# Performance work log

Measured on AMD Instinct MI355X. Metric: run time of the kernel, lower is better.

Reference implementation:

```python
import jax, jax.numpy as jnp
import numpy as np


def setup_inputs() -> dict:
    key0 = jax.random.key(0)
    kq, kk, kv = jax.random.split(key0, 3)
    B, H, L, S, D = 2, 8, 2048, 2048, 64
    query = jax.random.normal(kq, (B, H, L, D), dtype=jnp.float32)
    key = jax.random.normal(kk, (B, H, S, D), dtype=jnp.float32)
    value = jax.random.normal(kv, (B, H, S, D), dtype=jnp.float32)
    return {"query": query, "key": key, "value": value}


def reference(query, key, value):
    # Original computes matmul(q[b,h,l,1,d,1], k[b,h,1,s,1,d]) -> [B,H,L,S,D,D]
    # outer products, divides by sqrt(query.shape[-1]) AFTER unsqueeze (==1, no-op),
    # then sums dims (4,5). That is algebraically exactly rowsum(q)*rowsum(k).
    qsum = query.sum(axis=-1)                       # [B,H,L]
    ksum = key.sum(axis=-1)                         # [B,H,S]
    score = qsum[..., :, None] * ksum[..., None, :]  # [B,H,L,S]
    attn = jax.nn.softmax(score, axis=-1)            # softmax over S
    out = jnp.einsum('bhls,bhsd->bhld', attn, value)  # [B,H,L,D]
    return out
```

## Files before the change

kernel.cpp:

```cpp
#include <hip/hip_runtime.h>
#include <hip/hip_bf16.h>

#define BH 16
#define L 2048
#define S 2048
#define DD 64
#define BM 64
#define BK 64
#define LDSPAD 8
#define LDW (BK + LDSPAD)

typedef __attribute__((ext_vector_type(4))) float f32x4;
typedef __bf16 bf16x8 __attribute__((ext_vector_type(8)));

union FragU {
  bf16x8 f;
  __hip_bfloat162 h2[4];
};

__device__ inline __hip_bfloat162 exp2pack(float al2, float nsl2, float k0,
                                           float k1, float& d) {
  float e0 = __builtin_amdgcn_exp2f(fmaf(al2, k0, nsl2));
  float e1 = __builtin_amdgcn_exp2f(fmaf(al2, k1, nsl2));
  d += e0 + e1;
  return __float22bfloat162_rn(make_float2(e0, e1));
}

__global__ __launch_bounds__(256) void prep_kernel(
    const float* __restrict__ k, const float* __restrict__ v,
    float* __restrict__ ks, __hip_bfloat16* __restrict__ vt) {
  __shared__ __hip_bfloat16 tile[DD][LDW];
  int t = threadIdx.x;
  if (blockIdx.x < 2048) {
    int g = blockIdx.x * 256 + t;
    int row = g >> 4;
    int l16 = g & 15;
    float4 x = reinterpret_cast<const float4*>(k + (size_t)row * DD)[l16];
    float s = x.x + x.y + x.z + x.w;
    s += __shfl_xor(s, 1);
    s += __shfl_xor(s, 2);
    s += __shfl_xor(s, 4);
    s += __shfl_xor(s, 8);
    if (l16 == 0) ks[row] = s;
  } else {
    int bid = blockIdx.x - 2048;
    int s0 = (bid & 31) * 64;
    int bh = bid >> 5;
    int srow = t >> 4;
    int d4 = (t & 15) * 4;
#pragma unroll
    for (int kk = 0; kk < 4; ++kk) {
      int s = srow + kk * 16;
      float4 val = *reinterpret_cast<const float4*>(
          v + ((size_t)(bh * S + s0 + s)) * DD + d4);
      tile[d4 + 0][s] = __float2bfloat16(val.x);
      tile[d4 + 1][s] = __float2bfloat16(val.y);
      tile[d4 + 2][s] = __float2bfloat16(val.z);
      tile[d4 + 3][s] = __float2bfloat16(val.w);
    }
    __syncthreads();
    int dd = t >> 3;
    int j = t & 7;
#pragma unroll
    for (int kk = 0; kk < 2; ++kk) {
      int d = dd + kk * 32;
      uint4 val = *reinterpret_cast<const uint4*>(&tile[d][j * 8]);
      *reinterpret_cast<uint4*>(vt + ((size_t)(bh * DD + d)) * S + s0 + j * 8) =
          val;
    }
  }
}

__global__ __launch_bounds__(256) void attn_kernel(
    const float* __restrict__ q, const __hip_bfloat16* __restrict__ vt,
    const float* __restrict__ ks, float* __restrict__ out) {
  int l0 = blockIdx.x * BM;
  int bh = blockIdx.y;

  __shared__ __hip_bfloat16 ldsVT[2][DD][LDW];
  __shared__ float a_row[BM];
  __shared__ float red[16];

  int t = threadIdx.x;
  int lane = t & 63;
  int w = t >> 6;
  int m = lane & 15;
  int qd = lane >> 4;

  const __hip_bfloat16* vtb = vt + (size_t)bh * DD * S;
  const float* ksb = ks + (size_t)bh * S;

  int vd = t >> 3;
  int vj = t & 7;

  uint4 v0 = *reinterpret_cast<const uint4*>(vtb + (size_t)vd * S + vj * 8);
  uint4 v1 =
      *reinterpret_cast<const uint4*>(vtb + (size_t)(vd + 32) * S + vj * 8);
  float4 kA0 = *reinterpret_cast<const float4*>(ksb + qd * 8);
  float4 kA1 = *reinterpret_cast<const float4*>(ksb + qd * 8 + 4);
  float4 kB0 = *reinterpret_cast<const float4*>(ksb + 32 + qd * 8);
  float4 kB1 = *reinterpret_cast<const float4*>(ksb + 32 + qd * 8 + 4);

  {
    int r = t >> 2;
    int p = t & 3;
    const float* qp = q + ((size_t)(bh * L + l0 + r)) * DD + p * 16;
    float4 x0 = reinterpret_cast<const float4*>(qp)[0];
    float4 x1 = reinterpret_cast<const float4*>(qp)[1];
    float4 x2 = reinterpret_cast<const float4*>(qp)[2];
    float4 x3 = reinterpret_cast<const float4*>(qp)[3];
    float s = (x0.x + x0.y + x0.z + x0.w) + (x1.x + x1.y + x1.z + x1.w) +
              (x2.x + x2.y + x2.z + x2.w) + (x3.x + x3.y + x3.z + x3.w);
    s += __shfl_xor(s, 1);
    s += __shfl_xor(s, 2);
    if (p == 0) a_row[r] = s;
  }

  {
    const float* kp = ksb + t * 8;
    float4 y0 = reinterpret_cast<const float4*>(kp)[0];
    float4 y1 = reinterpret_cast<const float4*>(kp)[1];
    float mx = fmaxf(fmaxf(fmaxf(y0.x, y0.y), fmaxf(y0.z, y0.w)),
                     fmaxf(fmaxf(y1.x, y1.y), fmaxf(y1.z, y1.w)));
    float mn = fminf(fminf(fminf(y0.x, y0.y), fminf(y0.z, y0.w)),
                     fminf(fminf(y1.x, y1.y), fminf(y1.z, y1.w)));
#pragma unroll
    for (int off = 1; off < 64; off <<= 1) {
      mx = fmaxf(mx, __shfl_xor(mx, off));
      mn = fminf(mn, __shfl_xor(mn, off));
    }
    if (lane == 0) {
      red[w] = mx;
      red[8 + w] = mn;
    }
  }
  __syncthreads();

  float kmax = fmaxf(fmaxf(red[0], red[1]), fmaxf(red[2], red[3]));
  float kmin = fminf(fminf(red[8], red[9]), fminf(red[10], red[11]));
  float ar = a_row[w * 16 + m];
  float sel = (ar > 0.f) ? kmax : kmin;
  const float LOG2E = 1.44269504088896f;
  float al2 = ar * LOG2E;
  float nsl2 = -al2 * sel;

  float dsum = 0.f;
  f32x4 acc[4];
#pragma unroll
  for (int c = 0; c < 4; ++c) acc[c] = (f32x4){0.f, 0.f, 0.f, 0.f};

  for (int it = 0; it < 32; ++it) {
    int bufi = it & 1;
    *reinterpret_cast<uint4*>(&ldsVT[bufi][vd][vj * 8]) = v0;
    *reinterpret_cast<uint4*>(&ldsVT[bufi][vd + 32][vj * 8]) = v1;
    __syncthreads();

    int s0n = (it < 31) ? (it + 1) * BK : 31 * BK;
    v0 = *reinterpret_cast<const uint4*>(vtb + (size_t)vd * S + s0n + vj * 8);
    v1 = *reinterpret_cast<const uint4*>(vtb + (size_t)(vd + 32) * S + s0n +
                                         vj * 8);

    FragU f0, f1;
    f0.h2[0] = exp2pack(al2, nsl2, kA0.x, kA0.y, dsum);
    f0.h2[1] = exp2pack(al2, nsl2, kA0.z, kA0.w, dsum);
    f0.h2[2] = exp2pack(al2, nsl2, kA1.x, kA1.y, dsum);
    f0.h2[3] = exp2pack(al2, nsl2, kA1.z, kA1.w, dsum);
    f1.h2[0] = exp2pack(al2, nsl2, kB0.x, kB0.y, dsum);
    f1.h2[1] = exp2pack(al2, nsl2, kB0.z, kB0.w, dsum);
    f1.h2[2] = exp2pack(al2, nsl2, kB1.x, kB1.y, dsum);
    f1.h2[3] = exp2pack(al2, nsl2, kB1.z, kB1.w, dsum);

    kA0 = *reinterpret_cast<const float4*>(ksb + s0n + qd * 8);
    kA1 = *reinterpret_cast<const float4*>(ksb + s0n + qd * 8 + 4);
    kB0 = *reinterpret_cast<const float4*>(ksb + s0n + 32 + qd * 8);
    kB1 = *reinterpret_cast<const float4*>(ksb + s0n + 32 + qd * 8 + 4);

#pragma unroll
    for (int c = 0; c < 4; ++c) {
      uint4 bu0 =
          *reinterpret_cast<const uint4*>(&ldsVT[bufi][c * 16 + m][qd * 8]);
      acc[c] = __builtin_amdgcn_mfma_f32_16x16x32_bf16(
          f0.f, __builtin_bit_cast(bf16x8, bu0), acc[c], 0, 0, 0);
      uint4 bu1 = *reinterpret_cast<const uint4*>(
          &ldsVT[bufi][c * 16 + m][32 + qd * 8]);
      acc[c] = __builtin_amdgcn_mfma_f32_16x16x32_bf16(
          f1.f, __builtin_bit_cast(bf16x8, bu1), acc[c], 0, 0, 0);
    }
  }

  float dt = dsum;
  dt += __shfl_xor(dt, 16);
  dt += __shfl_xor(dt, 32);
  float inv[4];
#pragma unroll
  for (int i = 0; i < 4; ++i) inv[i] = 1.0f / __shfl(dt, qd * 4 + i);

  float* ob = out + ((size_t)(bh * L + l0 + w * 16)) * DD;
#pragma unroll
  for (int c = 0; c < 4; ++c) {
#pragma unroll
    for (int i = 0; i < 4; ++i) {
      ob[(size_t)(qd * 4 + i) * DD + c * 16 + m] = acc[c][i] * inv[i];
    }
  }
}

extern "C" void kernel_launch(void* const* d_in, const int* in_sizes, int n_in,
                              void* d_out, int out_size, void* d_ws,
                              size_t ws_size, hipStream_t stream) {
  const float* q = (const float*)d_in[0];
  const float* k = (const float*)d_in[1];
  const float* v = (const float*)d_in[2];
  float* out = (float*)d_out;
  float* ws = (float*)d_ws;

  float* ks = ws;
  __hip_bfloat16* vt = (__hip_bfloat16*)(ws + BH * S);

  prep_kernel<<<2048 + 512, 256, 0, stream>>>(k, v, ks, vt);
  attn_kernel<<<dim3(L / BM, BH), 256, 0, stream>>>(q, vt, ks, out);
}
```

Before: 97.35 us.

## Split S across waves in 512-thread blocks, compute denominators via MFMA, reduce in LDS

The attention kernel now runs 512 threads, organised as 2 row groups by 4 S-slices. Each wave computes 32 rows (two 16-row fragments) over its own S slice, so each V fragment loaded from LDS is reused twice. The loop runs 8 steps of 256 S instead of 32 steps of 64, which cuts the number of barriers. The softmax denominator is now accumulated with MFMAs against a ones vector rather than scalar adds. Partial outputs and denominators are then combined across S-slice waves through LDS, which adds a reduction epilogue and more LDS traffic in exchange.

```diff
diff --git a/kernel.cpp b/kernel.cpp
--- a/kernel.cpp
+++ b/kernel.cpp
@@ -18,11 +18,12 @@
   __hip_bfloat162 h2[4];
 };
 
-__device__ inline __hip_bfloat162 exp2pack(float al2, float nsl2, float k0,
-                                           float k1, float& d) {
+#define MFMA16(a, b, c) __builtin_amdgcn_mfma_f32_16x16x32_bf16((a), (b), (c), 0, 0, 0)
+
+__device__ inline __hip_bfloat162 exp2pk(float al2, float nsl2, float k0,
+                                         float k1) {
   float e0 = __builtin_amdgcn_exp2f(fmaf(al2, k0, nsl2));
   float e1 = __builtin_amdgcn_exp2f(fmaf(al2, k1, nsl2));
-  d += e0 + e1;
   return __float22bfloat162_rn(make_float2(e0, e1));
 }
 
@@ -71,59 +72,65 @@
   }
 }
 
-__global__ __launch_bounds__(256) void attn_kernel(
+__global__ __launch_bounds__(512, 4) void attn_kernel(
     const float* __restrict__ q, const __hip_bfloat16* __restrict__ vt,
     const float* __restrict__ ks, float* __restrict__ out) {
   int l0 = blockIdx.x * BM;
   int bh = blockIdx.y;
 
-  __shared__ __hip_bfloat16 ldsVT[2][DD][LDW];
+  __shared__ char smem[2 * 4 * DD * LDW * 2] __attribute__((aligned(16)));
   __shared__ float a_row[BM];
   __shared__ float red[16];
+  __shared__ float drow[4][2][2][16];
+
+  auto ldsVT = reinterpret_cast<__hip_bfloat16(*)[4][DD][LDW]>(smem);
+  auto cmb = reinterpret_cast<float(*)[32][65]>(smem);
 
   int t = threadIdx.x;
   int lane = t & 63;
   int w = t >> 6;
+  int rg = w >> 2;
+  int sg = w & 3;
   int m = lane & 15;
   int qd = lane >> 4;
 
   const __hip_bfloat16* vtb = vt + (size_t)bh * DD * S;
   const float* ksb = ks + (size_t)bh * S;
 
-  int vd = t >> 3;
-  int vj = t & 7;
-
-  uint4 v0 = *reinterpret_cast<const uint4*>(vtb + (size_t)vd * S + vj * 8);
-  uint4 v1 =
-      *reinterpret_cast<const uint4*>(vtb + (size_t)(vd + 32) * S + vj * 8);
-  float4 kA0 = *reinterpret_cast<const float4*>(ksb + qd * 8);
-  float4 kA1 = *reinterpret_cast<const float4*>(ksb + qd * 8 + 4);
-  float4 kB0 = *reinterpret_cast<const float4*>(ksb + 32 + qd * 8);
-  float4 kB1 = *reinterpret_cast<const float4*>(ksb + 32 + qd * 8 + 4);
+  int tg = t >> 7;
+  int u = t & 127;
+  int vd = u >> 1;
+  int vh = u & 1;
+
+  const __hip_bfloat16* vs0 =
+      vtb + (size_t)vd * S + tg * 64 + vh * 32;
+  uint4 p0 = reinterpret_cast<const uint4*>(vs0)[0];
+  uint4 p1 = reinterpret_cast<const uint4*>(vs0)[1];
+  uint4 p2 = reinterpret_cast<const uint4*>(vs0)[2];
+  uint4 p3 = reinterpret_cast<const uint4*>(vs0)[3];
+  int kb0 = sg * 64;
+  float4 kA0 = *reinterpret_cast<const float4*>(ksb + kb0 + qd * 8);
+  float4 kA1 = *reinterpret_cast<const float4*>(ksb + kb0 + qd * 8 + 4);
+  float4 kB0 = *reinterpret_cast<const float4*>(ksb + kb0 + 32 + qd * 8);
+  float4 kB1 = *reinterpret_cast<const float4*>(ksb + kb0 + 32 + qd * 8 + 4);
 
   {
-    int r = t >> 2;
-    int p = t & 3;
-    const float* qp = q + ((size_t)(bh * L + l0 + r)) * DD + p * 16;
+    int r = t >> 3;
+    int p = t & 7;
+    const float* qp = q + ((size_t)(bh * L + l0 + r)) * DD + p * 8;
     float4 x0 = reinterpret_cast<const float4*>(qp)[0];
     float4 x1 = reinterpret_cast<const float4*>(qp)[1];
-    float4 x2 = reinterpret_cast<const float4*>(qp)[2];
-    float4 x3 = reinterpret_cast<const float4*>(qp)[3];
-    float s = (x0.x + x0.y + x0.z + x0.w) + (x1.x + x1.y + x1.z + x1.w) +
-              (x2.x + x2.y + x2.z + x2.w) + (x3.x + x3.y + x3.z + x3.w);
+    float s = (x0.x + x0.y + x0.z + x0.w) + (x1.x + x1.y + x1.z + x1.w);
     s += __shfl_xor(s, 1);
     s += __shfl_xor(s, 2);
+    s += __shfl_xor(s, 4);
     if (p == 0) a_row[r] = s;
   }
 
   {
-    const float* kp = ksb + t * 8;
-    float4 y0 = reinterpret_cast<const float4*>(kp)[0];
-    float4 y1 = reinterpret_cast<const float4*>(kp)[1];
-    float mx = fmaxf(fmaxf(fmaxf(y0.x, y0.y), fmaxf(y0.z, y0.w)),
-                     fmaxf(fmaxf(y1.x, y1.y), fmaxf(y1.z, y1.w)));
-    float mn = fminf(fminf(fminf(y0.x, y0.y), fminf(y0.z, y0.w)),
-                     fminf(fminf(y1.x, y1.y), fminf(y1.z, y1.w)));
+    float4 y = *reinterpret_cast<const float4*>(ksb + t * 4);
+    float mx = fmaxf(fmaxf(y.x, y.y), fmaxf(y.z, y.w));
+    float mn = fminf(fminf(y.x, y.y), fminf(y.z, y.w));
 #pragma unroll
     for (int off = 1; off < 64; off <<= 1) {
       mx = fmaxf(mx, __shfl_xor(mx, off));
@@ -134,74 +141,169 @@
       red[8 + w] = mn;
     }
   }
+
+  {
+    uint4* dst = reinterpret_cast<uint4*>(&ldsVT[0][tg][vd][vh * 32]);
+    dst[0] = p0;
+    dst[1] = p1;
+    dst[2] = p2;
+    dst[3] = p3;
+  }
   __syncthreads();
 
-  float kmax = fmaxf(fmaxf(red[0], red[1]), fmaxf(red[2], red[3]));
-  float kmin = fminf(fminf(red[8], red[9]), fminf(red[10], red[11]));
-  float ar = a_row[w * 16 + m];
-  float sel = (ar > 0.f) ? kmax : kmin;
+  float kmax = red[0], kmin = red[8];
+#pragma unroll
+  for (int i = 1; i < 8; ++i) {
+    kmax = fmaxf(kmax, red[i]);
+    kmin = fminf(kmin, red[8 + i]);
+  }
   const float LOG2E = 1.44269504088896f;
-  float al2 = ar * LOG2E;
-  float nsl2 = -al2 * sel;
-
-  float dsum = 0.f;
-  f32x4 acc[4];
-#pragma unroll
-  for (int c = 0; c < 4; ++c) acc[c] = (f32x4){0.f, 0.f, 0.f, 0.f};
-
-  for (int it = 0; it < 32; ++it) {
-    int bufi = it & 1;
-    *reinterpret_cast<uint4*>(&ldsVT[bufi][vd][vj * 8]) = v0;
-    *reinterpret_cast<uint4*>(&ldsVT[bufi][vd + 32][vj * 8]) = v1;
-    __syncthreads();
-
-    int s0n = (it < 31) ? (it + 1) * BK : 31 * BK;
-    v0 = *reinterpret_cast<const uint4*>(vtb + (size_t)vd * S + s0n + vj * 8);
-    v1 = *reinterpret_cast<const uint4*>(vtb + (size_t)(vd + 32) * S + s0n +
-                                         vj * 8);
-
-    FragU f0, f1;
-    f0.h2[0] = exp2pack(al2, nsl2, kA0.x, kA0.y, dsum);
-    f0.h2[1] = exp2pack(al2, nsl2, kA0.z, kA0.w, dsum);
-    f0.h2[2] = exp2pack(al2, nsl2, kA1.x, kA1.y, dsum);
-    f0.h2[3] = exp2pack(al2, nsl2, kA1.z, kA1.w, dsum);
-    f1.h2[0] = exp2pack(al2, nsl2, kB0.x, kB0.y, dsum);
-    f1.h2[1] = exp2pack(al2, nsl2, kB0.z, kB0.w, dsum);
-    f1.h2[2] = exp2pack(al2, nsl2, kB1.x, kB1.y, dsum);
-    f1.h2[3] = exp2pack(al2, nsl2, kB1.z, kB1.w, dsum);
-
-    kA0 = *reinterpret_cast<const float4*>(ksb + s0n + qd * 8);
-    kA1 = *reinterpret_cast<const float4*>(ksb + s0n + qd * 8 + 4);
-    kB0 = *reinterpret_cast<const float4*>(ksb + s0n + 32 + qd * 8);
-    kB1 = *reinterpret_cast<const float4*>(ksb + s0n + 32 + qd * 8 + 4);
+  float ar0 = a_row[rg * 32 + m];
+  float ar1 = a_row[rg * 32 + 16 + m];
+  float al2_0 = ar0 * LOG2E, al2_1 = ar1 * LOG2E;
+  float nsl2_0 = -al2_0 * ((ar0 > 0.f) ? kmax : kmin);
+  float nsl2_1 = -al2_1 * ((ar1 > 0.f) ? kmax : kmin);
+
+  FragU of;
+  {
+    __hip_bfloat162 one2 = __float22bfloat162_rn(make_float2(1.f, 1.f));
+    of.h2[0] = of.h2[1] = of.h2[2] = of.h2[3] = one2;
+  }
+
+  f32x4 acc0[4], acc1[4];
+  f32x4 ad0 = (f32x4){0.f, 0.f, 0.f, 0.f};
+  f32x4 ad1 = (f32x4){0.f, 0.f, 0.f, 0.f};
+#pragma unroll
+  for (int c = 0; c < 4; ++c) {
+    acc0[c] = (f32x4){0.f, 0.f, 0.f, 0.f};
+    acc1[c] = (f32x4){0.f, 0.f, 0.f, 0.f};
+  }
+
+  for (int step = 0; step < 8; ++step) {
+    int buf = step & 1;
+
+    int sn = (step < 7) ? step + 1 : 7;
+    const __hip_bfloat16* vs =
+        vtb + (size_t)vd * S + (sn * 4 + tg) * 64 + vh * 32;
+    uint4 n0 = reinterpret_cast<const uint4*>(vs)[0];
+    uint4 n1 = reinterpret_cast<const uint4*>(vs)[1];
+    uint4 n2 = reinterpret_cast<const uint4*>(vs)[2];
+    uint4 n3 = reinterpret_cast<const uint4*>(vs)[3];
+
+    FragU fA0, fA1, fB0, fB1;
+    fA0.h2[0] = exp2pk(al2_0, nsl2_0, kA0.x, kA0.y);
+    fA0.h2[1] = exp2pk(al2_0, nsl2_0, kA0.z, kA0.w);
+    fA0.h2[2] = exp2pk(al2_0, nsl2_0, kA1.x, kA1.y);
+    fA0.h2[3] = exp2pk(al2_0, nsl2_0, kA1.z, kA1.w);
+    fA1.h2[0] = exp2pk(al2_0, nsl2_0, kB0.x, kB0.y);
+    fA1.h2[1] = exp2pk(al2_0, nsl2_0, kB0.z, kB0.w);
+    fA1.h2[2] = exp2pk(al2_0, nsl2_0, kB1.x, kB1.y);
+    fA1.h2[3] = exp2pk(al2_0, nsl2_0, kB1.z, kB1.w);
+    fB0.h2[0] = exp2pk(al2_1, nsl2_1, kA0.x, kA0.y);
+    fB0.h2[1] = exp2pk(al2_1, nsl2_1, kA0.z, kA0.w);
+    fB0.h2[2] = exp2pk(al2_1, nsl2_1, kA1.x, kA1.y);
+    fB0.h2[3] = exp2pk(al2_1, nsl2_1, kA1.z, kA1.w);
+    fB1.h2[0] = exp2pk(al2_1, nsl2_1, kB0.x, kB0.y);
+    fB1.h2[1] = exp2pk(al2_1, nsl2_1, kB0.z, kB0.w);
+    fB1.h2[2] = exp2pk(al2_1, nsl2_1, kB1.x, kB1.y);
+    fB1.h2[3] = exp2pk(al2_1, nsl2_1, kB1.z, kB1.w);
+
+    int kbn = ((step < 7) ? (step + 1) * 4 + sg : 28 + sg) * 64;
+    kA0 = *reinterpret_cast<const float4*>(ksb + kbn + qd * 8);
+    kA1 = *reinterpret_cast<const float4*>(ksb + kbn + qd * 8 + 4);
+    kB0 = *reinterpret_cast<const float4*>(ksb + kbn + 32 + qd * 8);
+    kB1 = *reinterpret_cast<const float4*>(ksb + kbn + 32 + qd * 8 + 4);
+
+    ad0 = MFMA16(fA0.f, of.f, ad0);
+    ad0 = MFMA16(fA1.f, of.f, ad0);
+    ad1 = MFMA16(fB0.f, of.f, ad1);
+    ad1 = MFMA16(fB1.f, of.f, ad1);
 
 #pragma unroll
     for (int c = 0; c < 4; ++c) {
-      uint4 bu0 =
-          *reinterpret_cast<const uint4*>(&ldsVT[bufi][c * 16 + m][qd * 8]);
-      acc[c] = __builtin_amdgcn_mfma_f32_16x16x32_bf16(
-          f0.f, __builtin_bit_cast(bf16x8, bu0), acc[c], 0, 0, 0);
-      uint4 bu1 = *reinterpret_cast<const uint4*>(
-          &ldsVT[bufi][c * 16 + m][32 + qd * 8]);
-      acc[c] = __builtin_amdgcn_mfma_f32_16x16x32_bf16(
-          f1.f, __builtin_bit_cast(bf16x8, bu1), acc[c], 0, 0, 0);
-    }
-  }
-
-  float dt = dsum;
-  dt += __shfl_xor(dt, 16);
-  dt += __shfl_xor(dt, 32);
-  float inv[4];
-#pragma unroll
-  for (int i = 0; i < 4; ++i) inv[i] = 1.0f / __shfl(dt, qd * 4 + i);
-
-  float* ob = out + ((size_t)(bh * L + l0 + w * 16)) * DD;
-#pragma unroll
-  for (int c = 0; c < 4; ++c) {
+      uint4 b0 =
+          *reinterpret_cast<const uint4*>(&ldsVT[buf][sg][c * 16 + m][qd * 8]);
+      bf16x8 bb0 = __builtin_bit_cast(bf16x8, b0);
+      acc0[c] = MFMA16(fA0.f, bb0, acc0[c]);
+      acc1[c] = MFMA16(fB0.f, bb0, acc1[c]);
+      uint4 b1 = *reinterpret_cast<const uint4*>(
+          &ldsVT[buf][sg][c * 16 + m][32 + qd * 8]);
+      bf16x8 bb1 = __builtin_bit_cast(bf16x8, b1);
+      acc0[c] = MFMA16(fA1.f, bb1, acc0[c]);
+      acc1[c] = MFMA16(fB1.f, bb1, acc1[c]);
+    }
+
+    if (step < 7) {
+      uint4* dst =
+          reinterpret_cast<uint4*>(&ldsVT[(step + 1) & 1][tg][vd][vh * 32]);
+      dst[0] = n0;
+      dst[1] = n1;
+      dst[2] = n2;
+      dst[3] = n3;
+      __syncthreads();
+    }
+  }
+
+  if (m == 0) {
 #pragma unroll
     for (int i = 0; i < 4; ++i) {
-      ob[(size_t)(qd * 4 + i) * DD + c * 16 + m] = acc[c][i] * inv[i];
-    }
+      drow[sg][rg][0][qd * 4 + i] = ad0[i];
+      drow[sg][rg][1][qd * 4 + i] = ad1[i];
+    }
+  }
+  if (sg >= 2) {
+    int z = rg * 2 + (sg - 2);
+#pragma unroll
+    for (int c = 0; c < 4; ++c)
+#pragma unroll
+      for (int i = 0; i < 4; ++i) {
+        cmb[z][qd * 4 + i][c * 16 + m] = acc0[c][i];
+        cmb[z][16 + qd * 4 + i][c * 16 + m] = acc1[c][i];
+      }
+  }
+  __syncthreads();
+  if (sg < 2) {
+    int z = rg * 2 + sg;
+#pragma unroll
+    for (int c = 0; c < 4; ++c)
+#pragma unroll
+      for (int i = 0; i < 4; ++i) {
+        acc0[c][i] += cmb[z][qd * 4 + i][c * 16 + m];
+        acc1[c][i] += cmb[z][16 + qd * 4 + i][c * 16 + m];
+      }
+  }
+  if (sg == 1) {
+    int z = rg * 2 + 1;
+#pragma unroll
+    for (int c = 0; c < 4; ++c)
+#pragma unroll
+      for (int i = 0; i < 4; ++i) {
+        cmb[z][qd * 4 + i][c * 16 + m] = acc0[c][i];
+        cmb[z][16 + qd * 4 + i][c * 16 + m] = acc1[c][i];
+      }
+  }
+  __syncthreads();
+  if (sg == 0) {
+    int z = rg * 2 + 1;
+    float inv0[4], inv1[4];
+#pragma unroll
+    for (int i = 0; i < 4; ++i) {
+      int r = qd * 4 + i;
+      inv0[i] = 1.0f / (drow[0][rg][0][r] + drow[1][rg][0][r] +
+                        drow[2][rg][0][r] + drow[3][rg][0][r]);
+      inv1[i] = 1.0f / (drow[0][rg][1][r] + drow[1][rg][1][r] +
+                        drow[2][rg][1][r] + drow[3][rg][1][r]);
+    }
+    float* ob = out + ((size_t)(bh * L + l0 + rg * 32)) * DD;
+#pragma unroll
+    for (int c = 0; c < 4; ++c)
+#pragma unroll
+      for (int i = 0; i < 4; ++i) {
+        float t0 = acc0[c][i] + cmb[z][qd * 4 + i][c * 16 + m];
+        float t1 = acc1[c][i] + cmb[z][16 + qd * 4 + i][c * 16 + m];
+        ob[(size_t)(qd * 4 + i) * DD + c * 16 + m] = t0 * inv0[i];
+        ob[(size_t)(16 + qd * 4 + i) * DD + c * 16 + m] = t1 * inv1[i];
+      }
   }
 }
 
@@ -218,5 +320,5 @@
   __hip_bfloat16* vt = (__hip_bfloat16*)(ws + BH * S);
 
   prep_kernel<<<2048 + 512, 256, 0, stream>>>(k, v, ks, vt);
-  attn_kernel<<<dim3(L / BM, BH), 256, 0, stream>>>(q, vt, ks, out);
+  attn_kernel<<<dim3(L / BM, BH), 512, 0, stream>>>(q, vt, ks, out);
 }
```

Result: faster. 93.90 us (-3.5%).
